# Performance work log

Measured on AMD Instinct MI355X. Metric: run time of the kernel, lower is better.

Reference implementation:

```python
import jax, jax.numpy as jnp
import numpy as np

C = 256          # in_channels
DEPTH = 2        # iters
DIM_HEAD = 16    # groups g (since in_channels not in {32,64,128})
HEAD_DIM = C // DIM_HEAD   # channels per group = hidden_dim = 16
SCALE = HEAD_DIM ** -0.5
BN_EPS = 1e-5


def setup_inputs() -> dict:
    key = jax.random.key(0)
    ks = jax.random.split(key, 20)
    B, H, W = 8, 128, 128
    s = 0.05
    inp = {
        'x': jax.random.normal(ks[0], (B, C, H, W), dtype=jnp.float32),
        # q/k/v 1x1 conv weights (torch Conv2d weight [out,in,1,1] -> [out,in])
        'Wq': jax.random.normal(ks[1], (C, C), dtype=jnp.float32) * s,
        'Wk': jax.random.normal(ks[2], (C, C), dtype=jnp.float32) * s,
        'Wv': jax.random.normal(ks[3], (C, C), dtype=jnp.float32) * s,
        'bv': jax.random.normal(ks[4], (C,), dtype=jnp.float32) * s,
        # BatchNorm (eval mode) params for q and k branches
        'gq': 1.0 + jax.random.normal(ks[5], (C,), dtype=jnp.float32) * s,
        'bq': jax.random.normal(ks[6], (C,), dtype=jnp.float32) * s,
        'mq': jax.random.normal(ks[7], (C,), dtype=jnp.float32) * s,
        'vq': jax.random.uniform(ks[8], (C,), dtype=jnp.float32, minval=0.5, maxval=1.5),
        'gk': 1.0 + jax.random.normal(ks[9], (C,), dtype=jnp.float32) * s,
        'bk': jax.random.normal(ks[10], (C,), dtype=jnp.float32) * s,
        'mk': jax.random.normal(ks[11], (C,), dtype=jnp.float32) * s,
        'vk': jax.random.uniform(ks[12], (C,), dtype=jnp.float32, minval=0.5, maxval=1.5),
        # MLP head: Linear(dim_head -> hidden_dim) -> GELU -> Linear(hidden_dim -> dim_head)
        'W1': jax.random.normal(ks[13], (DIM_HEAD, HEAD_DIM), dtype=jnp.float32) * s,
        'b1': jax.random.normal(ks[14], (HEAD_DIM,), dtype=jnp.float32) * s,
        'W2': jax.random.normal(ks[15], (HEAD_DIM, DIM_HEAD), dtype=jnp.float32) * s,
        'b2': jax.random.normal(ks[16], (DIM_HEAD,), dtype=jnp.float32) * s,
        # output fusion conv: 2C -> C, with bias
        'Wd': jax.random.normal(ks[17], (C, 2 * C), dtype=jnp.float32) * s,
        'bd': jax.random.normal(ks[18], (C,), dtype=jnp.float32) * s,
    }
    return inp


def _conv1x1(x, W):
    # x: [B,C,H,W], W: [O,C]
    return jnp.einsum('bchw,oc->bohw', x, W)


def _bn(x, g, b, m, v):
    inv = g * jax.lax.rsqrt(v + BN_EPS)
    return x * inv[None, :, None, None] + (b - m * inv)[None, :, None, None]


def reference(x, Wq, Wk, Wv, bv, gq, bq, mq, vq, gk, bk, mk, vk,
              W1, b1, W2, b2, Wd, bd):
    B, Cc, H, Wdim = x.shape
    g, c = DIM_HEAD, Cc // DIM_HEAD
    L = H * Wdim
    x0 = x
    for _ in range(DEPTH):
        q = _bn(_conv1x1(x, Wq), gq, bq, mq, vq)
        k = _bn(_conv1x1(x, Wk), gk, bk, mk, vk)
        v = _conv1x1(x, Wv) + bv[None, :, None, None]
        # unfold(kernel=1) is identity: [B,C,H,W] -> [B,g,c,1,L]
        q = q.reshape(B, g, c, 1, L)
        k = k.reshape(B, g, c, 1, L)
        v = v.reshape(B, g, c, 1, L)
        # attention over the (singleton) window dim i
        attn = jnp.einsum('bgcil,bgcml->bgiml', k, q) * SCALE
        attn = jax.nn.softmax(attn, axis=2)
        o = jnp.einsum('bgiml,bgcil->bgcml', attn, v)  # [B,g,c,1,L]
        # transpose(1,4): MLP acts over the group dim g (size dim_head)
        o = o.transpose(0, 4, 2, 3, 1)  # [B,L,c,1,g]
        h = jax.nn.gelu(o @ W1 + b1, approximate=False)  # dropout off (eval)
        o = h @ W2 + b2
        o = o.transpose(0, 4, 2, 3, 1).reshape(B, Cc, H, Wdim)
        x = o
    out = jnp.concatenate([x0, x], axis=1)  # [B,2C,H,W]
    return _conv1x1(out, Wd) + bd[None, :, None, None]
```

## Files before the change

kernel.cpp:

```cpp
#include <hip/hip_runtime.h>


typedef short v8s __attribute__((ext_vector_type(8)));
typedef float v4f __attribute__((ext_vector_type(4)));

#define L_   16384
#define PIX  32

__device__ __forceinline__ unsigned short bf16rne(float f) {
  union { float f; unsigned u; } v; v.f = f;
  unsigned u = v.u;
  return (unsigned short)((u + 0x7FFFu + ((u >> 16) & 1u)) >> 16);
}

__device__ __forceinline__ unsigned cvt_pk_bf16(float lo, float hi) {
  unsigned r;
  asm("v_cvt_pk_bf16_f32 %0, %1, %2" : "=v"(r) : "v"(lo), "v"(hi));
  return r;
}

__device__ __forceinline__ float gelu_fast(float x) {
  float y = 1.5957691216057308f * (x + 0.044715f * x * x * x);
  float e = __expf(y);
  float t = 1.0f - 2.0f / (e + 1.0f);
  return 0.5f * x * (1.0f + t);
}


__global__ void prep_pack_k(const float* __restrict__ Wv, const float* __restrict__ W1,
                            const float* __restrict__ W2, const float* __restrict__ Wd,
                            unsigned short* __restrict__ pA1, unsigned short* __restrict__ pG3,
                            float* __restrict__ T) {
  int gtid = blockIdx.x * 256 + threadIdx.x;
  int seg = gtid >> 16;
  int tid = gtid & 65535;
  if (seg == 3) {
    int c = tid & 15, jj = (tid >> 4) & 15, cp = (tid >> 8) & 15, g = tid >> 12;
    float s = 0.f;
    for (int j2 = 0; j2 < 16; ++j2)
      s += Wv[(g * 16 + cp) * 256 + j2 * 16 + c] * W2[jj * 16 + j2];
    T[tid] = s;
    return;
  }
  int j = tid & 7, lane = (tid >> 3) & 63, kt = (tid >> 9) & 7, mt = tid >> 12;
  int m = mt * 16 + (lane & 15);
  int k = kt * 32 + (lane >> 4) * 8 + j;
  if (seg == 0) {
    pG3[((mt * 16 + kt) * 64 + lane) * 8 + j] = bf16rne(Wd[m * 512 + k]);
  } else if (seg == 1) {
    int jj = k >> 4, c = k & 15;
    float s = 0.f;
    for (int j2 = 0; j2 < 16; ++j2)
      s += Wd[m * 512 + 256 + j2 * 16 + c] * W2[jj * 16 + j2];
    pG3[((mt * 16 + 8 + kt) * 64 + lane) * 8 + j] = bf16rne(s);
  } else {
    int jp = m >> 4, c = m & 15;
    float s = 0.f;
    for (int g = 0; g < 16; ++g) s += W1[g * 16 + jp] * Wv[(g * 16 + c) * 256 + k];
    pA1[tid] = bf16rne(s);
  }
}

__global__ void prep_a12_k(const float* __restrict__ W1, const float* __restrict__ T,
                           unsigned short* __restrict__ dst) {
  int tid = blockIdx.x * 256 + threadIdx.x;
  int j = tid & 7, lane = (tid >> 3) & 63, kt = (tid >> 9) & 7, mt = tid >> 12;
  int m = mt * 16 + (lane & 15);
  int k = kt * 32 + (lane >> 4) * 8 + j;
  int jp = m >> 4, cp = m & 15;
  int jj = k >> 4, c = k & 15;
  float s = 0.f;
  for (int g = 0; g < 16; ++g)
    s += W1[g * 16 + jp] * T[g * 4096 + cp * 256 + jj * 16 + c];
  dst[tid] = bf16rne(s);
}

__global__ void prep_bias_k(const float* __restrict__ Wv, const float* __restrict__ bv,
                            const float* __restrict__ Wd, const float* __restrict__ W1,
                            const float* __restrict__ b1, const float* __restrict__ b2,
                            const float* __restrict__ bd,
                            float* __restrict__ b1p, float* __restrict__ b12p,
                            float* __restrict__ bdp) {
  __shared__ float tmp[256];
  int h = threadIdx.x;
  {
    int g = h >> 4, cp = h & 15;
    float s = bv[g * 16 + cp];
    for (int j2 = 0; j2 < 16; ++j2) {
      float b2v = b2[j2];
      for (int c = 0; c < 16; ++c) s += Wv[(g * 16 + cp) * 256 + j2 * 16 + c] * b2v;
    }
    tmp[h] = s;
    float sd = bd[h];
    for (int j2 = 0; j2 < 16; ++j2) {
      float b2v = b2[j2];
      for (int c = 0; c < 16; ++c) sd += Wd[h * 512 + 256 + j2 * 16 + c] * b2v;
    }
    bdp[h] = sd;
  }
  __syncthreads();
  {
    int j = h >> 4, c = h & 15;
    float s1 = b1[j], s2 = b1[j];
    for (int g = 0; g < 16; ++g) {
      float w = W1[g * 16 + j];
      s1 += w * bv[g * 16 + c];
      s2 += w * tmp[g * 16 + c];
    }
    b1p[h] = s1;
    b12p[h] = s2;
  }
}


__device__ __forceinline__ v8s bfrag(const short* __restrict__ S, int nt, int kt,
                                     int l15, int quad) {
  int p = nt * 16 + l15;
  int g = (kt * 4 + quad) ^ (p & 7);
  return *(const v8s*)&S[p * 256 + g * 8];
}

__device__ __forceinline__ void gemm8(const unsigned short* __restrict__ packA,
                                      const short* __restrict__ S,
                                      int w, int lane, int l15, int quad,
                                      v4f acc[4][2]) {
  const unsigned short* pa = packA + w * 16384 + lane * 8;
  v8s a_cur[4], a_nxt[4], b_cur[2], b_nxt[2];
#pragma unroll
  for (int mi = 0; mi < 4; ++mi) a_cur[mi] = *(const v8s*)(pa + mi * 8 * 512);
  b_cur[0] = bfrag(S, 0, 0, l15, quad);
  b_cur[1] = bfrag(S, 1, 0, l15, quad);
#pragma unroll
  for (int kt = 0; kt < 8; ++kt) {
    if (kt < 7) {
#pragma unroll
      for (int mi = 0; mi < 4; ++mi)
        a_nxt[mi] = *(const v8s*)(pa + (mi * 8 + kt + 1) * 512);
      b_nxt[0] = bfrag(S, 0, kt + 1, l15, quad);
      b_nxt[1] = bfrag(S, 1, kt + 1, l15, quad);
    }
#pragma unroll
    for (int mi = 0; mi < 4; ++mi) {
      acc[mi][0] = __builtin_amdgcn_mfma_f32_16x16x32_bf16(a_cur[mi], b_cur[0], acc[mi][0], 0, 0, 0);
      acc[mi][1] = __builtin_amdgcn_mfma_f32_16x16x32_bf16(a_cur[mi], b_cur[1], acc[mi][1], 0, 0, 0);
    }
#pragma unroll
    for (int mi = 0; mi < 4; ++mi) a_cur[mi] = a_nxt[mi];
    b_cur[0] = b_nxt[0];
    b_cur[1] = b_nxt[1];
  }
}

__device__ __forceinline__ void epi(v4f acc[4][2], const float* __restrict__ bias,
                                    short* __restrict__ HB, int w, int l15, int quad) {
#pragma unroll
  for (int mi = 0; mi < 4; ++mi) {
    int rb = (w * 4 + mi) * 16 + quad * 4;
    float b0 = bias[rb], b1v = bias[rb + 1], b2v = bias[rb + 2], b3v = bias[rb + 3];
#pragma unroll
    for (int nt = 0; nt < 2; ++nt) {
      int p = nt * 16 + l15;
      float g0 = gelu_fast(acc[mi][nt][0] + b0);
      float g1 = gelu_fast(acc[mi][nt][1] + b1v);
      float g2 = gelu_fast(acc[mi][nt][2] + b2v);
      float g3 = gelu_fast(acc[mi][nt][3] + b3v);
      uint2 u;
      u.x = cvt_pk_bf16(g0, g1);
      u.y = cvt_pk_bf16(g2, g3);
      int g = (rb >> 3) ^ (p & 7);
      *(uint2*)&HB[p * 256 + g * 8 + (rb & 7)] = u;
      acc[mi][nt] = (v4f){0.f, 0.f, 0.f, 0.f};
    }
  }
}

__global__ __launch_bounds__(256, 4) void fused_k(
    const float* __restrict__ x,
    const unsigned short* __restrict__ pA1, const unsigned short* __restrict__ pA12,
    const unsigned short* __restrict__ pG3,
    const float* __restrict__ b1p, const float* __restrict__ b12p,
    const float* __restrict__ bdp, float* __restrict__ out) {
  __shared__ __align__(16) short XB[PIX * 256];
  __shared__ __align__(16) short HB[PIX * 256];
  const int t = threadIdx.x;
  const int lane = t & 63, w = t >> 6;
  const int quad = lane >> 4, l15 = lane & 15;
  const int pp0 = blockIdx.x * PIX;
  const int b = pp0 >> 14, l0 = pp0 & 16383;
  const float* xb = x + ((long)b << 22) + l0;

  {
    const int pq = t & 7, co = t >> 3;
    const int p0 = pq * 4;
    v4f v[8];
#pragma unroll
    for (int u = 0; u < 8; ++u)
      v[u] = *(const v4f*)(xb + (long)(co * 8 + u) * L_ + p0);
#pragma unroll
    for (int j = 0; j < 4; ++j) {
      const int p = p0 + j;
      uint4 s;
      s.x = cvt_pk_bf16(v[0][j], v[1][j]);
      s.y = cvt_pk_bf16(v[2][j], v[3][j]);
      s.z = cvt_pk_bf16(v[4][j], v[5][j]);
      s.w = cvt_pk_bf16(v[6][j], v[7][j]);
      *(uint4*)&XB[p * 256 + (co ^ (p & 7)) * 8] = s;
    }
  }

  v4f acc[4][2];
#pragma unroll
  for (int i = 0; i < 4; ++i) {
    acc[i][0] = (v4f){0.f, 0.f, 0.f, 0.f};
    acc[i][1] = (v4f){0.f, 0.f, 0.f, 0.f};
  }

  __syncthreads();

  gemm8(pA1, XB, w, lane, l15, quad, acc);
  epi(acc, b1p, HB, w, l15, quad);
  __syncthreads();
  gemm8(pA12, HB, w, lane, l15, quad, acc);
  __syncthreads();
  epi(acc, b12p, HB, w, l15, quad);
  __syncthreads();

  {
    const unsigned short* pg = pG3 + w * 32768 + lane * 8;
    v8s a_cur[4], a_nxt[4], b_cur[2], b_nxt[2];
#pragma unroll
    for (int mi = 0; mi < 4; ++mi) a_cur[mi] = *(const v8s*)(pg + mi * 16 * 512);
    b_cur[0] = bfrag(XB, 0, 0, l15, quad);
    b_cur[1] = bfrag(XB, 1, 0, l15, quad);
#pragma unroll
    for (int kt = 0; kt < 16; ++kt) {
      if (kt < 15) {
        const short* Sn = (kt + 1 < 8) ? XB : HB;
        const int ktl = (kt + 1) & 7;
#pragma unroll
        for (int mi = 0; mi < 4; ++mi)
          a_nxt[mi] = *(const v8s*)(pg + (mi * 16 + kt + 1) * 512);
        b_nxt[0] = bfrag(Sn, 0, ktl, l15, quad);
        b_nxt[1] = bfrag(Sn, 1, ktl, l15, quad);
      }
#pragma unroll
      for (int mi = 0; mi < 4; ++mi) {
        acc[mi][0] = __builtin_amdgcn_mfma_f32_16x16x32_bf16(a_cur[mi], b_cur[0], acc[mi][0], 0, 0, 0);
        acc[mi][1] = __builtin_amdgcn_mfma_f32_16x16x32_bf16(a_cur[mi], b_cur[1], acc[mi][1], 0, 0, 0);
      }
#pragma unroll
      for (int mi = 0; mi < 4; ++mi) a_cur[mi] = a_nxt[mi];
      b_cur[0] = b_nxt[0];
      b_cur[1] = b_nxt[1];
    }
  }

  long obase = ((long)b << 22) + l0;
#pragma unroll
  for (int mi = 0; mi < 4; ++mi) {
    int rb = (w * 4 + mi) * 16 + quad * 4;
    float bb0 = bdp[rb], bb1 = bdp[rb + 1], bb2 = bdp[rb + 2], bb3 = bdp[rb + 3];
#pragma unroll
    for (int nt = 0; nt < 2; ++nt) {
      int p = nt * 16 + l15;
      out[obase + (long)(rb + 0) * L_ + p] = acc[mi][nt][0] + bb0;
      out[obase + (long)(rb + 1) * L_ + p] = acc[mi][nt][1] + bb1;
      out[obase + (long)(rb + 2) * L_ + p] = acc[mi][nt][2] + bb2;
      out[obase + (long)(rb + 3) * L_ + p] = acc[mi][nt][3] + bb3;
    }
  }
}


extern "C" void kernel_launch(void* const* d_in, const int* in_sizes, int n_in,
                              void* d_out, int out_size, void* d_ws, size_t ws_size,
                              hipStream_t stream) {
  const float* x  = (const float*)d_in[0];
  const float* Wv = (const float*)d_in[3];
  const float* bv = (const float*)d_in[4];
  const float* W1 = (const float*)d_in[13];
  const float* b1 = (const float*)d_in[14];
  const float* W2 = (const float*)d_in[15];
  const float* b2 = (const float*)d_in[16];
  const float* Wd = (const float*)d_in[17];
  const float* bd = (const float*)d_in[18];
  float* out = (float*)d_out;

  char* ws = (char*)d_ws;
  unsigned short* pA1  = (unsigned short*)(ws + 0);
  unsigned short* pA12 = (unsigned short*)(ws + 131072);
  unsigned short* pG3  = (unsigned short*)(ws + 262144);
  float* b1p  = (float*)(ws + 524288);
  float* b12p = (float*)(ws + 525312);
  float* bdp  = (float*)(ws + 526336);
  float* T    = (float*)(ws + 527360);

  prep_pack_k<<<1024, 256, 0, stream>>>(Wv, W1, W2, Wd, pA1, pG3, T);
  prep_a12_k <<<256, 256, 0, stream>>>(W1, T, pA12);
  prep_bias_k<<<1, 256, 0, stream>>>(Wv, bv, Wd, W1, b1, b2, bd, b1p, b12p, bdp);

  fused_k<<<4096, 256, 0, stream>>>(x, pA1, pA12, pG3, b1p, b12p, bdp, out);
}
```

Before: 375.1 us.

## Double pixel tile to 64 with 8 waves and reshape per-wave MFMA tiling

The pixel tile per block doubles from 32 to 64 and the block grows to 512 threads (8 waves). Each wave now covers 2 M-tiles by 4 N-tiles instead of 4 by 2, so every packed weight fragment loaded from global memory feeds twice as many pixels. This halves the grid and cuts repeated weight-fragment traffic per pixel. In exchange it doubles LDS per block (XB and HB), asks for 512-thread occupancy under launch_bounds(512,4), and needs more LDS reads for B fragments per MFMA.

Result: faster. 346.9 us (-7.5%).

```diff
diff --git a/kernel.cpp b/kernel.cpp
--- a/kernel.cpp
+++ b/kernel.cpp
@@ -5,7 +5,7 @@
 typedef float v4f __attribute__((ext_vector_type(4)));
 
 #define L_   16384
-#define PIX  32
+#define PIX  64
 
 __device__ __forceinline__ unsigned short bf16rne(float f) {
   union { float f; unsigned u; } v; v.f = f;
@@ -123,42 +123,42 @@
 __device__ __forceinline__ void gemm8(const unsigned short* __restrict__ packA,
                                       const short* __restrict__ S,
                                       int w, int lane, int l15, int quad,
-                                      v4f acc[4][2]) {
-  const unsigned short* pa = packA + w * 16384 + lane * 8;
-  v8s a_cur[4], a_nxt[4], b_cur[2], b_nxt[2];
-#pragma unroll
-  for (int mi = 0; mi < 4; ++mi) a_cur[mi] = *(const v8s*)(pa + mi * 8 * 512);
-  b_cur[0] = bfrag(S, 0, 0, l15, quad);
-  b_cur[1] = bfrag(S, 1, 0, l15, quad);
+                                      v4f acc[2][4]) {
+  const unsigned short* pa = packA + w * 2 * 8 * 512 + lane * 8;
+  v8s a_cur[2], a_nxt[2], b_cur[4], b_nxt[4];
+#pragma unroll
+  for (int mi = 0; mi < 2; ++mi) a_cur[mi] = *(const v8s*)(pa + mi * 8 * 512);
+#pragma unroll
+  for (int nt = 0; nt < 4; ++nt) b_cur[nt] = bfrag(S, nt, 0, l15, quad);
 #pragma unroll
   for (int kt = 0; kt < 8; ++kt) {
     if (kt < 7) {
 #pragma unroll
-      for (int mi = 0; mi < 4; ++mi)
+      for (int mi = 0; mi < 2; ++mi)
         a_nxt[mi] = *(const v8s*)(pa + (mi * 8 + kt + 1) * 512);
-      b_nxt[0] = bfrag(S, 0, kt + 1, l15, quad);
-      b_nxt[1] = bfrag(S, 1, kt + 1, l15, quad);
-    }
-#pragma unroll
-    for (int mi = 0; mi < 4; ++mi) {
-      acc[mi][0] = __builtin_amdgcn_mfma_f32_16x16x32_bf16(a_cur[mi], b_cur[0], acc[mi][0], 0, 0, 0);
-      acc[mi][1] = __builtin_amdgcn_mfma_f32_16x16x32_bf16(a_cur[mi], b_cur[1], acc[mi][1], 0, 0, 0);
-    }
-#pragma unroll
-    for (int mi = 0; mi < 4; ++mi) a_cur[mi] = a_nxt[mi];
-    b_cur[0] = b_nxt[0];
-    b_cur[1] = b_nxt[1];
-  }
-}
-
-__device__ __forceinline__ void epi(v4f acc[4][2], const float* __restrict__ bias,
+#pragma unroll
+      for (int nt = 0; nt < 4; ++nt) b_nxt[nt] = bfrag(S, nt, kt + 1, l15, quad);
+    }
+#pragma unroll
+    for (int mi = 0; mi < 2; ++mi)
+#pragma unroll
+      for (int nt = 0; nt < 4; ++nt)
+        acc[mi][nt] = __builtin_amdgcn_mfma_f32_16x16x32_bf16(a_cur[mi], b_cur[nt], acc[mi][nt], 0, 0, 0);
+#pragma unroll
+    for (int mi = 0; mi < 2; ++mi) a_cur[mi] = a_nxt[mi];
+#pragma unroll
+    for (int nt = 0; nt < 4; ++nt) b_cur[nt] = b_nxt[nt];
+  }
+}
+
+__device__ __forceinline__ void epi(v4f acc[2][4], const float* __restrict__ bias,
                                     short* __restrict__ HB, int w, int l15, int quad) {
 #pragma unroll
-  for (int mi = 0; mi < 4; ++mi) {
-    int rb = (w * 4 + mi) * 16 + quad * 4;
+  for (int mi = 0; mi < 2; ++mi) {
+    int rb = (w * 2 + mi) * 16 + quad * 4;
     float b0 = bias[rb], b1v = bias[rb + 1], b2v = bias[rb + 2], b3v = bias[rb + 3];
 #pragma unroll
-    for (int nt = 0; nt < 2; ++nt) {
+    for (int nt = 0; nt < 4; ++nt) {
       int p = nt * 16 + l15;
       float g0 = gelu_fast(acc[mi][nt][0] + b0);
       float g1 = gelu_fast(acc[mi][nt][1] + b1v);
@@ -174,7 +174,7 @@
   }
 }
 
-__global__ __launch_bounds__(256, 4) void fused_k(
+__global__ __launch_bounds__(512, 4) void fused_k(
     const float* __restrict__ x,
     const unsigned short* __restrict__ pA1, const unsigned short* __restrict__ pA12,
     const unsigned short* __restrict__ pG3,
@@ -190,7 +190,7 @@
   const float* xb = x + ((long)b << 22) + l0;
 
   {
-    const int pq = t & 7, co = t >> 3;
+    const int pq = t & 15, co = t >> 4;
     const int p0 = pq * 4;
     v4f v[8];
 #pragma unroll
@@ -204,16 +204,16 @@
       s.y = cvt_pk_bf16(v[2][j], v[3][j]);
       s.z = cvt_pk_bf16(v[4][j], v[5][j]);
       s.w = cvt_pk_bf16(v[6][j], v[7][j]);
-      *(uint4*)&XB[p * 256 + (co ^ (p & 7)) * 8] = s;
-    }
-  }
-
-  v4f acc[4][2];
-#pragma unroll
-  for (int i = 0; i < 4; ++i) {
-    acc[i][0] = (v4f){0.f, 0.f, 0.f, 0.f};
-    acc[i][1] = (v4f){0.f, 0.f, 0.f, 0.f};
-  }
+      *(uint4*)&XB[p * 256 + ((co ^ (p & 7)) * 8)];
+      *(uint4*)&XB[p * 256 + ((co ^ (p & 7)) * 8)] = s;
+    }
+  }
+
+  v4f acc[2][4];
+#pragma unroll
+  for (int i = 0; i < 2; ++i)
+#pragma unroll
+    for (int n = 0; n < 4; ++n) acc[i][n] = (v4f){0.f, 0.f, 0.f, 0.f};
 
   __syncthreads();
 
@@ -226,42 +226,42 @@
   __syncthreads();
 
   {
-    const unsigned short* pg = pG3 + w * 32768 + lane * 8;
-    v8s a_cur[4], a_nxt[4], b_cur[2], b_nxt[2];
-#pragma unroll
-    for (int mi = 0; mi < 4; ++mi) a_cur[mi] = *(const v8s*)(pg + mi * 16 * 512);
-    b_cur[0] = bfrag(XB, 0, 0, l15, quad);
-    b_cur[1] = bfrag(XB, 1, 0, l15, quad);
+    const unsigned short* pg = pG3 + w * 2 * 16 * 512 + lane * 8;
+    v8s a_cur[2], a_nxt[2], b_cur[4], b_nxt[4];
+#pragma unroll
+    for (int mi = 0; mi < 2; ++mi) a_cur[mi] = *(const v8s*)(pg + mi * 16 * 512);
+#pragma unroll
+    for (int nt = 0; nt < 4; ++nt) b_cur[nt] = bfrag(XB, nt, 0, l15, quad);
 #pragma unroll
     for (int kt = 0; kt < 16; ++kt) {
       if (kt < 15) {
         const short* Sn = (kt + 1 < 8) ? XB : HB;
         const int ktl = (kt + 1) & 7;
 #pragma unroll
-        for (int mi = 0; mi < 4; ++mi)
+        for (int mi = 0; mi < 2; ++mi)
           a_nxt[mi] = *(const v8s*)(pg + (mi * 16 + kt + 1) * 512);
-        b_nxt[0] = bfrag(Sn, 0, ktl, l15, quad);
-        b_nxt[1] = bfrag(Sn, 1, ktl, l15, quad);
+#pragma unroll
+        for (int nt = 0; nt < 4; ++nt) b_nxt[nt] = bfrag(Sn, nt, ktl, l15, quad);
       }
 #pragma unroll
-      for (int mi = 0; mi < 4; ++mi) {
-        acc[mi][0] = __builtin_amdgcn_mfma_f32_16x16x32_bf16(a_cur[mi], b_cur[0], acc[mi][0], 0, 0, 0);
-        acc[mi][1] = __builtin_amdgcn_mfma_f32_16x16x32_bf16(a_cur[mi], b_cur[1], acc[mi][1], 0, 0, 0);
-      }
-#pragma unroll
-      for (int mi = 0; mi < 4; ++mi) a_cur[mi] = a_nxt[mi];
-      b_cur[0] = b_nxt[0];
-      b_cur[1] = b_nxt[1];
+      for (int mi = 0; mi < 2; ++mi)
+#pragma unroll
+        for (int nt = 0; nt < 4; ++nt)
+          acc[mi][nt] = __builtin_amdgcn_mfma_f32_16x16x32_bf16(a_cur[mi], b_cur[nt], acc[mi][nt], 0, 0, 0);
+#pragma unroll
+      for (int mi = 0; mi < 2; ++mi) a_cur[mi] = a_nxt[mi];
+#pragma unroll
+      for (int nt = 0; nt < 4; ++nt) b_cur[nt] = b_nxt[nt];
     }
   }
 
   long obase = ((long)b << 22) + l0;
 #pragma unroll
-  for (int mi = 0; mi < 4; ++mi) {
-    int rb = (w * 4 + mi) * 16 + quad * 4;
+  for (int mi = 0; mi < 2; ++mi) {
+    int rb = (w * 2 + mi) * 16 + quad * 4;
     float bb0 = bdp[rb], bb1 = bdp[rb + 1], bb2 = bdp[rb + 2], bb3 = bdp[rb + 3];
 #pragma unroll
-    for (int nt = 0; nt < 2; ++nt) {
+    for (int nt = 0; nt < 4; ++nt) {
       int p = nt * 16 + l15;
       out[obase + (long)(rb + 0) * L_ + p] = acc[mi][nt][0] + bb0;
       out[obase + (long)(rb + 1) * L_ + p] = acc[mi][nt][1] + bb1;
@@ -299,5 +299,5 @@
   prep_a12_k <<<256, 256, 0, stream>>>(W1, T, pA12);
   prep_bias_k<<<1, 256, 0, stream>>>(Wv, bv, Wd, W1, b1, b2, bd, b1p, b12p, bdp);
 
-  fused_k<<<4096, 256, 0, stream>>>(x, pA1, pA12, pG3, b1p, b12p, bdp, out);
-}
+  fused_k<<<2048, 512, 0, stream>>>(x, pA1, pA12, pG3, b1p, b12p, bdp, out);
+}
```
